# Performance work log

Hardware: AMD Instinct MI355X
Metric: run time of the kernel (lower is better)

The kernel has to match this reference:

```python
import jax, jax.numpy as jnp
import numpy as np

N, E = 12288, 196608
IN_DIM, HID, HEADS, EMB, K = 128, 256, 4, 16, 2
NEG_SLOPE = 0.2


def gat_layer(x, src, dst, W, a_s, a_d, b, heads, out_dim):
    # x: [N, Fin]; src/dst: [E'] (self-loops already appended)
    n = x.shape[0]
    h = (x @ W).reshape(n, heads, out_dim)                 # [N,H,F]
    alpha_src = jnp.einsum('nhf,hf->nh', h, a_s)           # [N,H]
    alpha_dst = jnp.einsum('nhf,hf->nh', h, a_d)
    e = jax.nn.leaky_relu(alpha_src[src] + alpha_dst[dst], NEG_SLOPE)  # [E,H]
    # softmax over incoming edges per destination node
    m = jax.ops.segment_max(e, dst, num_segments=n)
    ex = jnp.exp(e - m[dst])
    s = jax.ops.segment_sum(ex, dst, num_segments=n)
    alpha = ex / s[dst]                                    # [E,H]
    msg = h[src] * alpha[..., None]                        # [E,H,F]
    agg = jax.ops.segment_sum(msg, dst, num_segments=n)    # [N,H,F]
    return agg.reshape(n, heads * out_dim) + b


def setup_inputs() -> dict:
    key = jax.random.key(0)
    ks = jax.random.split(key, 16)
    x = jax.random.normal(ks[0], (N, IN_DIM), dtype=jnp.float32)
    edge_index = jax.random.randint(ks[1], (2, E), 0, N, dtype=jnp.int32)

    def glorot(k, shape):
        fan = shape[0] + shape[-1]
        return jax.random.normal(k, shape, dtype=jnp.float32) * jnp.sqrt(2.0 / fan)

    inp = {"x": x, "edge_index": edge_index}
    inp["W1"] = glorot(ks[2], (IN_DIM, HEADS * HID))
    inp["as1"] = glorot(ks[3], (HEADS, HID))
    inp["ad1"] = glorot(ks[4], (HEADS, HID))
    inp["b1"] = jnp.zeros((HEADS * HID,), jnp.float32)
    inp["W2"] = glorot(ks[5], (HEADS * HID, HEADS * HID))
    inp["as2"] = glorot(ks[6], (HEADS, HID))
    inp["ad2"] = glorot(ks[7], (HEADS, HID))
    inp["b2"] = jnp.zeros((HEADS * HID,), jnp.float32)
    # layer 3: 1024 -> 16, 1 head
    inp["W3"] = glorot(ks[8], (HEADS * HID, EMB))
    inp["as3"] = glorot(ks[9], (1, EMB))
    inp["ad3"] = glorot(ks[10], (1, EMB))
    inp["b3"] = jnp.zeros((EMB,), jnp.float32)
    inp["centers"] = jax.random.normal(ks[11], (K, EMB), dtype=jnp.float32)
    return inp


def reference(x, edge_index, W1, as1, ad1, b1, W2, as2, ad2, b2, W3, as3, ad3, b3, centers):
    n = x.shape[0]
    loop = jnp.arange(n, dtype=edge_index.dtype)
    src = jnp.concatenate([edge_index[0], loop])
    dst = jnp.concatenate([edge_index[1], loop])

    h = jax.nn.elu(gat_layer(x, src, dst, W1, as1, ad1, b1, HEADS, HID))
    h = jax.nn.elu(gat_layer(h, src, dst, W2, as2, ad2, b2, HEADS, HID))
    z = gat_layer(h, src, dst, W3, as3, ad3, b3, 1, EMB)   # [N,EMB]

    adj_recon = jax.nn.sigmoid(z @ z.T)                    # [N,N]

    # Student-t soft assignment
    d2 = jnp.sum((z[:, None, :] - centers[None, :, :]) ** 2, axis=2)  # [N,K]
    q = 1.0 / (1.0 + d2)
    q = q / jnp.sum(q, axis=1, keepdims=True)
    return z, adj_recon, q
```

## Files before the change

### kernel.cpp

```cpp
#include <hip/hip_runtime.h>
#include <hip/hip_bf16.h>
#include <math.h>

#define N_NODES 12288
#define N_EDGES 196608
#define EP_EDGES (N_EDGES + N_NODES)
#define HEADS 4
#define HID 256
#define FDIM 1024
#define EMB 16
#define NEG_SLOPE 0.2f

typedef __attribute__((ext_vector_type(8))) short short8;
typedef __attribute__((ext_vector_type(4))) float f32x4;

__device__ __forceinline__ unsigned short f2bf(float f) {
  unsigned int u = __float_as_uint(f);
  u = (u + 0x7FFFu + ((u >> 16) & 1u)) >> 16;
  return (unsigned short)u;
}
__device__ __forceinline__ float bf2f(unsigned short h) {
  return __uint_as_float(((unsigned int)h) << 16);
}

__device__ __forceinline__ void t_tile_hi(const float* __restrict__ W,
                                          unsigned short* __restrict__ Th,
                                          int K, int N, int k0, int n0,
                                          int t, float (*tile)[33]) {
  int rr = t >> 3, cc = (t & 7) * 4;
  float4 v = *reinterpret_cast<const float4*>(&W[(size_t)(k0 + rr) * N + n0 + cc]);
  tile[rr][cc + 0] = v.x; tile[rr][cc + 1] = v.y; tile[rr][cc + 2] = v.z; tile[rr][cc + 3] = v.w;
  __syncthreads();
  ushort4 h;
  h.x = f2bf(tile[cc + 0][rr]);
  h.y = f2bf(tile[cc + 1][rr]);
  h.z = f2bf(tile[cc + 2][rr]);
  h.w = f2bf(tile[cc + 3][rr]);
  *reinterpret_cast<ushort4*>(&Th[(size_t)(n0 + rr) * K + k0 + cc]) = h;
}

#define HIST_BLKS (EP_EDGES / 256)
__global__ __launch_bounds__(256) void k_hist_prep(const int* __restrict__ ei,
                                                   int* __restrict__ cnt,
                                                   const float* __restrict__ x,
                                                   unsigned short* __restrict__ xbf,
                                                   const float* __restrict__ W1,
                                                   unsigned short* __restrict__ w1tHi,
                                                   const float* __restrict__ W2,
                                                   unsigned short* __restrict__ w2tHi,
                                                   const float* __restrict__ as1,
                                                   const float* __restrict__ ad1,
                                                   float* __restrict__ wa,
                                                   const float* __restrict__ W3,
                                                   unsigned short* __restrict__ w3t) {
  __shared__ float tile[32][33];
  int b = blockIdx.x, t = threadIdx.x;
  if (b < HIST_BLKS) {
    int i = b * 256 + t;
    if (i < EP_EDGES) {
      int d = (i < N_EDGES) ? ei[N_EDGES + i] : (i - N_EDGES);
      atomicAdd(&cnt[d], 1);
    }
  } else if (b < HIST_BLKS + 1536) {
    int i = (b - HIST_BLKS) * 256 + t;
    float4 v = *reinterpret_cast<const float4*>(&x[(size_t)i * 4]);
    ushort4 h;
    h.x = f2bf(v.x); h.y = f2bf(v.y); h.z = f2bf(v.z); h.w = f2bf(v.w);
    *reinterpret_cast<ushort4*>(&xbf[(size_t)i * 4]) = h;
  } else if (b < HIST_BLKS + 1536 + 128) {
    int tt = b - HIST_BLKS - 1536;
    t_tile_hi(W1, w1tHi, 128, FDIM, (tt >> 5) * 32, (tt & 31) * 32, t, tile);
  } else if (b < HIST_BLKS + 1536 + 128 + 1024) {
    int tt = b - HIST_BLKS - 1536 - 128;
    t_tile_hi(W2, w2tHi, FDIM, FDIM, (tt >> 5) * 32, (tt & 31) * 32, t, tile);
  } else if (b == HIST_BLKS + 1536 + 128 + 1024) {
    for (int idx = t; idx < 1024; idx += 256) {
      int sd = idx >> 9, h = (idx >> 7) & 3, k = idx & 127;
      const float* av = sd ? ad1 : as1;
      float acc = 0.f;
      for (int f = 0; f < 256; ++f)
        acc = fmaf(W1[(size_t)k * FDIM + h * 256 + f], av[h * 256 + f], acc);
      wa[idx] = acc;
    }
  } else {
    for (int idx = t; idx < 16384; idx += 256) {
      int c = idx >> 10, k = idx & 1023;
      w3t[idx] = f2bf(W3[(size_t)k * 16 + c]);
    }
  }
}

__global__ __launch_bounds__(1024) void k_scan_alpha(const int* __restrict__ cnt,
                                                     int* __restrict__ row_ptr,
                                                     int* __restrict__ bsum,
                                                     const float* __restrict__ x,
                                                     const float* __restrict__ wa,
                                                     float* __restrict__ asrc,
                                                     float* __restrict__ adst) {
  __shared__ int sd[1024];
  int tid = threadIdx.x;
  if (blockIdx.x < 12) {
    int gid = blockIdx.x * 1024 + tid;
    int v = cnt[gid];
    sd[tid] = v;
    __syncthreads();
    for (int d = 1; d < 1024; d <<= 1) {
      int t2 = (tid >= d) ? sd[tid - d] : 0;
      __syncthreads();
      sd[tid] += t2;
      __syncthreads();
    }
    row_ptr[gid] = sd[tid] - v;
    if (tid == 1023) bsum[blockIdx.x] = sd[1023];
  } else {
    int id = (blockIdx.x - 12) * 1024 + tid;
    int n = id >> 2, h = id & 3;
    const float* wsv = wa + h * 128;
    const float* wdv = wa + 512 + h * 128;
    const float* xr = x + (size_t)n * 128;
    float accs = 0.f, accd = 0.f;
#pragma unroll
    for (int k = 0; k < 128; k += 4) {
      float4 xv = *reinterpret_cast<const float4*>(&xr[k]);
      float4 s4 = *reinterpret_cast<const float4*>(&wsv[k]);
      float4 d4 = *reinterpret_cast<const float4*>(&wdv[k]);
      accs = fmaf(xv.x, s4.x, fmaf(xv.y, s4.y, fmaf(xv.z, s4.z, fmaf(xv.w, s4.w, accs))));
      accd = fmaf(xv.x, d4.x, fmaf(xv.y, d4.y, fmaf(xv.z, d4.z, fmaf(xv.w, d4.w, accd))));
    }
    asrc[n * 4 + h] = accs;
    adst[n * 4 + h] = accd;
  }
}

__global__ void k_scan23(int* __restrict__ row_ptr, const int* __restrict__ bsum) {
  int gid = blockIdx.x * 256 + threadIdx.x;
  int blk = gid >> 10;
  int boffv = 0;
  for (int j = 0; j < blk; ++j) boffv += bsum[j];
  row_ptr[gid] += boffv;
  if (gid == 0) {
    int tot = 0;
    for (int j = 0; j < 12; ++j) tot += bsum[j];
    row_ptr[N_NODES] = tot;
  }
}

__global__ void k_scatter(const int* __restrict__ ei, const int* __restrict__ row_ptr,
                          int* __restrict__ cur, int* __restrict__ csr_src) {
  int i = blockIdx.x * 256 + threadIdx.x;
  if (i >= EP_EDGES) return;
  int s, d;
  if (i < N_EDGES) { s = ei[i]; d = ei[N_EDGES + i]; }
  else             { s = i - N_EDGES; d = s; }
  int pos = row_ptr[d] + atomicAdd(&cur[d], 1);
  csr_src[pos] = s;
}

__global__ __launch_bounds__(256) void k_aggx(const unsigned short* __restrict__ xbf,
                                              const float* __restrict__ asrc,
                                              const float* __restrict__ adst,
                                              const int* __restrict__ row_ptr,
                                              const int* __restrict__ csr_src,
                                              unsigned short* __restrict__ outHi) {
  int node = (blockIdx.x * 256 + threadIdx.x) >> 6;
  int lane = threadIdx.x & 63;
  int beg = row_ptr[node], end = row_ptr[node + 1];
  float4 adn = *reinterpret_cast<const float4*>(&adst[node * 4]);
  float m0 = -INFINITY, m1 = -INFINITY, m2 = -INFINITY, m3 = -INFINITY;
  float s0 = 0.f, s1 = 0.f, s2 = 0.f, s3 = 0.f;
  float a0x = 0.f, a0y = 0.f, a1x = 0.f, a1y = 0.f;
  float a2x = 0.f, a2y = 0.f, a3x = 0.f, a3y = 0.f;
  for (int e = beg; e < end; ++e) {
    int sidx = csr_src[e];
    float4 av = *reinterpret_cast<const float4*>(&asrc[sidx * 4]);
    ushort2 hu = *reinterpret_cast<const ushort2*>(&xbf[(size_t)sidx * 128 + lane * 2]);
    float hx = bf2f(hu.x), hy = bf2f(hu.y);
    float a, nm, sc, p;
    a = av.x + adn.x; a = a > 0.f ? a : NEG_SLOPE * a;
    nm = fmaxf(m0, a); sc = __expf(m0 - nm); p = __expf(a - nm); m0 = nm;
    s0 = s0 * sc + p; a0x = a0x * sc + p * hx; a0y = a0y * sc + p * hy;
    a = av.y + adn.y; a = a > 0.f ? a : NEG_SLOPE * a;
    nm = fmaxf(m1, a); sc = __expf(m1 - nm); p = __expf(a - nm); m1 = nm;
    s1 = s1 * sc + p; a1x = a1x * sc + p * hx; a1y = a1y * sc + p * hy;
    a = av.z + adn.z; a = a > 0.f ? a : NEG_SLOPE * a;
    nm = fmaxf(m2, a); sc = __expf(m2 - nm); p = __expf(a - nm); m2 = nm;
    s2 = s2 * sc + p; a2x = a2x * sc + p * hx; a2y = a2y * sc + p * hy;
    a = av.w + adn.w; a = a > 0.f ? a : NEG_SLOPE * a;
    nm = fmaxf(m3, a); sc = __expf(m3 - nm); p = __expf(a - nm); m3 = nm;
    s3 = s3 * sc + p; a3x = a3x * sc + p * hx; a3y = a3y * sc + p * hy;
  }
  size_t base = (size_t)node * 512 + lane * 2;
  ushort2 o;
  float inv;
  inv = 1.f / s0; o.x = f2bf(a0x * inv); o.y = f2bf(a0y * inv);
  *reinterpret_cast<ushort2*>(&outHi[base + 0 * 128]) = o;
  inv = 1.f / s1; o.x = f2bf(a1x * inv); o.y = f2bf(a1y * inv);
  *reinterpret_cast<ushort2*>(&outHi[base + 1 * 128]) = o;
  inv = 1.f / s2; o.x = f2bf(a2x * inv); o.y = f2bf(a2y * inv);
  *reinterpret_cast<ushort2*>(&outHi[base + 2 * 128]) = o;
  inv = 1.f / s3; o.x = f2bf(a3x * inv); o.y = f2bf(a3y * inv);
  *reinterpret_cast<ushort2*>(&outHi[base + 3 * 128]) = o;
}

template <int MODE>
__global__ __launch_bounds__(256) void k_gemm(const unsigned short* __restrict__ A,
                                              const unsigned short* __restrict__ B,
                                              unsigned short* __restrict__ Out,
                                              const float* __restrict__ bias,
                                              const float* __restrict__ a_s,
                                              const float* __restrict__ a_d,
                                              float* __restrict__ asrcP,
                                              float* __restrict__ adstP,
                                              int M, int N, int K, int lda) {
  __shared__ unsigned short sA[128 * 32], sB[128 * 32];
  const int tid = threadIdx.x;
  const int lane = tid & 63, wv = tid >> 6;
  const int row0 = blockIdx.y * 128, col0 = blockIdx.x * 128;
  const int mBase = (wv >> 1) * 64, nBase = (wv & 1) * 64;
  const int lane15 = lane & 15;
  const int aoff = (MODE == 1) ? (col0 >> 8) * 128 : 0;

  f32x4 acc[4][4];
#pragma unroll
  for (int m = 0; m < 4; ++m)
#pragma unroll
    for (int n = 0; n < 4; ++n) acc[m][n] = (f32x4){0.f, 0.f, 0.f, 0.f};

  int rS[2], cS[2], dS[2];
#pragma unroll
  for (int c = 0; c < 2; ++c) {
    int p = c * 4096 + tid * 16;
    int r = p >> 6, u = (p >> 4) & 3;
    int f = (r & 3) ^ ((r >> 2) & 3);
    rS[c] = r; cS[c] = (u ^ f) * 8; dS[c] = c * 2048 + tid * 8;
  }
  const int fR = (lane & 3) ^ ((lane >> 2) & 3);
  const int uprime = (((lane >> 4) ^ fR) * 8);

  for (int k0 = 0; k0 < K; k0 += 32) {
#pragma unroll
    for (int c = 0; c < 2; ++c) {
      size_t ga = (size_t)(row0 + rS[c]) * lda + aoff + k0 + cS[c];
      size_t gb = (size_t)(col0 + rS[c]) * K + k0 + cS[c];
      __builtin_amdgcn_global_load_lds((const __attribute__((address_space(1))) void*)(A + ga),
                                       (__attribute__((address_space(3))) void*)(sA + dS[c]), 16, 0, 0);
      __builtin_amdgcn_global_load_lds((const __attribute__((address_space(1))) void*)(B + gb),
                                       (__attribute__((address_space(3))) void*)(sB + dS[c]), 16, 0, 0);
    }
    __syncthreads();

    short8 a[4], b[4];
#pragma unroll
    for (int m = 0; m < 4; ++m) {
      int ia = (mBase + m * 16 + lane15) * 32 + uprime;
      a[m] = *reinterpret_cast<const short8*>(sA + ia);
      int ib = (nBase + m * 16 + lane15) * 32 + uprime;
      b[m] = *reinterpret_cast<const short8*>(sB + ib);
    }
#pragma unroll
    for (int m = 0; m < 4; ++m)
#pragma unroll
      for (int n = 0; n < 4; ++n)
        acc[m][n] = __builtin_amdgcn_mfma_f32_16x16x32_bf16(a[m], b[n], acc[m][n], 0, 0, 0);
    __syncthreads();
  }

  const int head = col0 >> 8;
  const int q = ((col0 >> 6) & 2) | (nBase >> 6);
  float asv[4], adv[4];
  if (MODE == 0) {
#pragma unroll
    for (int n = 0; n < 4; ++n) {
      int cc = col0 + nBase + n * 16 + lane15;
      asv[n] = a_s[cc];
      adv[n] = a_d[cc];
    }
  }

#pragma unroll
  for (int m = 0; m < 4; ++m) {
    int rr = row0 + mBase + m * 16 + (lane >> 4) * 4;
#pragma unroll
    for (int j = 0; j < 4; ++j) {
      if (MODE == 1) {
#pragma unroll
        for (int n = 0; n < 4; ++n) {
          int cc = col0 + nBase + n * 16 + lane15;
          float v = acc[m][n][j] + bias[cc];
          v = v > 0.f ? v : __expf(v) - 1.f;
          Out[(size_t)(rr + j) * N + cc] = f2bf(v);
        }
      } else {
        float ps = 0.f, pd = 0.f;
#pragma unroll
        for (int n = 0; n < 4; ++n) {
          int cc = col0 + nBase + n * 16 + lane15;
          float v = acc[m][n][j];
          Out[(size_t)(rr + j) * N + cc] = f2bf(v);
          ps = fmaf(v, asv[n], ps);
          pd = fmaf(v, adv[n], pd);
        }
        ps += __shfl_xor(ps, 1); pd += __shfl_xor(pd, 1);
        ps += __shfl_xor(ps, 2); pd += __shfl_xor(pd, 2);
        ps += __shfl_xor(ps, 4); pd += __shfl_xor(pd, 4);
        ps += __shfl_xor(ps, 8); pd += __shfl_xor(pd, 8);
        if (lane15 == 0) {
          asrcP[(size_t)(rr + j) * 16 + head * 4 + q] = ps;
          adstP[(size_t)(rr + j) * 16 + head * 4 + q] = pd;
        }
      }
    }
  }
}

__global__ __launch_bounds__(256) void k_agg4(const unsigned short* __restrict__ h,
                                              const float* __restrict__ asrcP,
                                              const float* __restrict__ adstP,
                                              const int* __restrict__ row_ptr,
                                              const int* __restrict__ csr_src, const float* __restrict__ bias,
                                              unsigned short* __restrict__ outHi) {
  int wid = (blockIdx.x * 256 + threadIdx.x) >> 6;
  int lane = threadIdx.x & 63;
  int node = wid >> 2, hd = wid & 3;
  int beg = row_ptr[node], end = row_ptr[node + 1];
  float4 dq = *reinterpret_cast<const float4*>(&adstP[(size_t)node * 16 + hd * 4]);
  float adn = dq.x + dq.y + dq.z + dq.w;
  float m = -INFINITY, s = 0.f;
  float ax = 0.f, ay = 0.f, az = 0.f, aw = 0.f;
  for (int e = beg; e < end; ++e) {
    int sidx = csr_src[e];
    float4 sq = *reinterpret_cast<const float4*>(&asrcP[(size_t)sidx * 16 + hd * 4]);
    float a = (sq.x + sq.y + sq.z + sq.w) + adn;
    a = a > 0.f ? a : NEG_SLOPE * a;
    float nm = fmaxf(m, a);
    float sc = __expf(m - nm);
    float p  = __expf(a - nm);
    m = nm;
    s = s * sc + p;
    ushort4 hu = *reinterpret_cast<const ushort4*>(&h[(size_t)sidx * FDIM + hd * HID + lane * 4]);
    ax = ax * sc + p * bf2f(hu.x);
    ay = ay * sc + p * bf2f(hu.y);
    az = az * sc + p * bf2f(hu.z);
    aw = aw * sc + p * bf2f(hu.w);
  }
  float inv = 1.f / s;
  int fo = hd * HID + lane * 4;
  float4 bv = *reinterpret_cast<const float4*>(&bias[fo]);
  float4 o;
  o.x = ax * inv + bv.x; o.y = ay * inv + bv.y; o.z = az * inv + bv.z; o.w = aw * inv + bv.w;
  o.x = o.x > 0.f ? o.x : __expf(o.x) - 1.f;
  o.y = o.y > 0.f ? o.y : __expf(o.y) - 1.f;
  o.z = o.z > 0.f ? o.z : __expf(o.z) - 1.f;
  o.w = o.w > 0.f ? o.w : __expf(o.w) - 1.f;
  ushort4 hh;
  hh.x = f2bf(o.x); hh.y = f2bf(o.y); hh.z = f2bf(o.z); hh.w = f2bf(o.w);
  *reinterpret_cast<ushort4*>(&outHi[(size_t)node * FDIM + fo]) = hh;
}

__global__ __launch_bounds__(256) void k_gemm_n16(const unsigned short* __restrict__ A,
                                                  const unsigned short* __restrict__ w3t,
                                                  const float* __restrict__ a_s,
                                                  const float* __restrict__ a_d,
                                                  float* __restrict__ C,
                                                  float* __restrict__ asrc,
                                                  float* __restrict__ adst) {
  int wave = (blockIdx.x * 256 + threadIdx.x) >> 6;
  int lane = threadIdx.x & 63;
  int lane15 = lane & 15;
  int row0 = wave * 16;
  int kg = (lane >> 4) * 8;
  f32x4 acc = (f32x4){0.f, 0.f, 0.f, 0.f};
  const unsigned short* Ar = A + (size_t)(row0 + lane15) * FDIM + kg;
  const unsigned short* Br = w3t + (size_t)lane15 * FDIM + kg;
  for (int k0 = 0; k0 < FDIM; k0 += 32) {
    short8 a = *reinterpret_cast<const short8*>(Ar + k0);
    short8 b = *reinterpret_cast<const short8*>(Br + k0);
    acc = __builtin_amdgcn_mfma_f32_16x16x32_bf16(a, b, acc, 0, 0, 0);
  }
  float asv = a_s[lane15], adv = a_d[lane15];
  int rbase = row0 + (lane >> 4) * 4;
#pragma unroll
  for (int j = 0; j < 4; ++j) {
    float v = acc[j];
    C[(size_t)(rbase + j) * EMB + lane15] = v;
    float ps = v * asv, pd = v * adv;
    ps += __shfl_xor(ps, 1); pd += __shfl_xor(pd, 1);
    ps += __shfl_xor(ps, 2); pd += __shfl_xor(pd, 2);
    ps += __shfl_xor(ps, 4); pd += __shfl_xor(pd, 4);
    ps += __shfl_xor(ps, 8); pd += __shfl_xor(pd, 8);
    if (lane15 == 0) { asrc[rbase + j] = ps; adst[rbase + j] = pd; }
  }
}

__global__ __launch_bounds__(256) void k_agg1(const float* __restrict__ h3, const float* __restrict__ asrc,
                                              const float* __restrict__ adst, const int* __restrict__ row_ptr,
                                              const int* __restrict__ csr_src, const float* __restrict__ bias,
                                              const float* __restrict__ centers,
                                              float* __restrict__ z, float* __restrict__ qout) {
  int idx = blockIdx.x * 256 + threadIdx.x;
  int node = idx >> 4, f = idx & 15;
  if (node >= N_NODES) return;
  int beg = row_ptr[node], end = row_ptr[node + 1];
  float adn = adst[node];
  float m = -INFINITY, s = 0.f, acc = 0.f;
  for (int e = beg; e < end; ++e) {
    int sidx = csr_src[e];
    float a = asrc[sidx] + adn;
    a = a > 0.f ? a : NEG_SLOPE * a;
    float nm = fmaxf(m, a);
    float sc = __expf(m - nm);
    float p  = __expf(a - nm);
    m = nm;
    s = s * sc + p;
    acc = acc * sc + p * h3[sidx * EMB + f];
  }
  float zv = acc / s + bias[f];
  z[node * EMB + f] = zv;
  float d0 = zv - centers[f];       d0 *= d0;
  float d1 = zv - centers[EMB + f]; d1 *= d1;
  d0 += __shfl_xor(d0, 1); d1 += __shfl_xor(d1, 1);
  d0 += __shfl_xor(d0, 2); d1 += __shfl_xor(d1, 2);
  d0 += __shfl_xor(d0, 4); d1 += __shfl_xor(d1, 4);
  d0 += __shfl_xor(d0, 8); d1 += __shfl_xor(d1, 8);
  if (f == 0) {
    float q0 = 1.f / (1.f + d0), q1 = 1.f / (1.f + d1);
    float inv = 1.f / (q0 + q1);
    qout[node * 2 + 0] = q0 * inv;
    qout[node * 2 + 1] = q1 * inv;
  }
}

__global__ __launch_bounds__(256) void k_adj(const float* __restrict__ z, float* __restrict__ adj) {
  __shared__ float Zr[16][64];
  __shared__ float Zc[16][64];
  int tid = threadIdx.x;
  int r0 = blockIdx.y * 64, c0 = blockIdx.x * 64;
  {
    int m = tid >> 2, kk = (tid & 3) * 4;
    float4 v = *reinterpret_cast<const float4*>(&z[(size_t)(r0 + m) * EMB + kk]);
    Zr[kk + 0][m] = v.x; Zr[kk + 1][m] = v.y; Zr[kk + 2][m] = v.z; Zr[kk + 3][m] = v.w;
    float4 w = *reinterpret_cast<const float4*>(&z[(size_t)(c0 + m) * EMB + kk]);
    Zc[kk + 0][m] = w.x; Zc[kk + 1][m] = w.y; Zc[kk + 2][m] = w.z; Zc[kk + 3][m] = w.w;
  }
  __syncthreads();
  int tx = tid & 15, ty = tid >> 4;
  float acc[4][4] = {};
#pragma unroll
  for (int k = 0; k < 16; ++k) {
    float a[4], b[4];
#pragma unroll
    for (int i = 0; i < 4; ++i) a[i] = Zr[k][ty * 4 + i];
#pragma unroll
    for (int j = 0; j < 4; ++j) b[j] = Zc[k][tx * 4 + j];
#pragma unroll
    for (int i = 0; i < 4; ++i)
#pragma unroll
      for (int j = 0; j < 4; ++j) acc[i][j] = fmaf(a[i], b[j], acc[i][j]);
  }
  for (int i = 0; i < 4; ++i) {
    float4 o;
    o.x = 1.f / (1.f + __expf(-acc[i][0]));
    o.y = 1.f / (1.f + __expf(-acc[i][1]));
    o.z = 1.f / (1.f + __expf(-acc[i][2]));
    o.w = 1.f / (1.f + __expf(-acc[i][3]));
    *reinterpret_cast<float4*>(&adj[(size_t)(r0 + ty * 4 + i) * N_NODES + c0 + tx * 4]) = o;
  }
}

extern "C" void kernel_launch(void* const* d_in, const int* in_sizes, int n_in,
                              void* d_out, int out_size, void* d_ws, size_t ws_size,
                              hipStream_t stream) {
  const float* x   = (const float*)d_in[0];
  const int*   ei  = (const int*)d_in[1];
  const float* W1  = (const float*)d_in[2];
  const float* as1 = (const float*)d_in[3];
  const float* ad1 = (const float*)d_in[4];
  const float* b1  = (const float*)d_in[5];
  const float* W2  = (const float*)d_in[6];
  const float* as2 = (const float*)d_in[7];
  const float* ad2 = (const float*)d_in[8];
  const float* b2  = (const float*)d_in[9];
  const float* W3  = (const float*)d_in[10];
  const float* as3 = (const float*)d_in[11];
  const float* ad3 = (const float*)d_in[12];
  const float* b3  = (const float*)d_in[13];
  const float* centers = (const float*)d_in[14];
  float* out = (float*)d_out;

  char* ws = (char*)d_ws;
  size_t off = 0;
  auto alloc = [&](size_t bytes) { void* p = ws + off; off = (off + bytes + 255) & ~(size_t)255; return p; };
  int* cnt       = (int*)alloc((size_t)N_NODES * 4);
  int* cur       = (int*)alloc((size_t)N_NODES * 4);
  int* row_ptr   = (int*)alloc((size_t)(N_NODES + 1) * 4);
  int* bsum      = (int*)alloc(64 * 4);
  int* csr_src   = (int*)alloc((size_t)EP_EDGES * 4);
  float* asrcA   = (float*)alloc((size_t)N_NODES * HEADS * 4);
  float* adstA   = (float*)alloc((size_t)N_NODES * HEADS * 4);
  float* asrcP   = (float*)alloc((size_t)N_NODES * 16 * 4);
  float* adstP   = (float*)alloc((size_t)N_NODES * 16 * 4);
  float* asrc3   = (float*)alloc((size_t)N_NODES * 4);
  float* adst3   = (float*)alloc((size_t)N_NODES * 4);
  float* wa      = (float*)alloc(1024 * 4);
  unsigned short* xbf    = (unsigned short*)alloc((size_t)N_NODES * 128 * 2);
  unsigned short* aggxHi = (unsigned short*)alloc((size_t)N_NODES * 512 * 2);
  unsigned short* h1bf   = (unsigned short*)alloc((size_t)N_NODES * FDIM * 2);
  unsigned short* hbf    = (unsigned short*)alloc((size_t)N_NODES * FDIM * 2);
  unsigned short* agg2Hi = (unsigned short*)alloc((size_t)N_NODES * FDIM * 2);
  unsigned short* w1tHi  = (unsigned short*)alloc((size_t)FDIM * 128 * 2);
  unsigned short* w2tHi  = (unsigned short*)alloc((size_t)FDIM * FDIM * 2);
  unsigned short* w3t    = (unsigned short*)alloc((size_t)16 * FDIM * 2);
  float* bufZ    = (float*)alloc((size_t)N_NODES * EMB * 4);

  hipMemsetAsync(cnt, 0, (size_t)N_NODES * 8, stream);

  k_hist_prep<<<dim3(HIST_BLKS + 1536 + 128 + 1024 + 2), dim3(256), 0, stream>>>(
      ei, cnt, x, xbf, W1, w1tHi, W2, w2tHi, as1, ad1, wa, W3, w3t);

  k_scan_alpha<<<dim3(12 + 48), dim3(1024), 0, stream>>>(
      cnt, row_ptr, bsum, x, wa, asrcA, adstA);

  k_scan23<<<dim3(N_NODES / 256), dim3(256), 0, stream>>>(row_ptr, bsum);
  k_scatter<<<dim3((EP_EDGES + 255) / 256), dim3(256), 0, stream>>>(ei, row_ptr, cur, csr_src);

  k_aggx<<<dim3(N_NODES / 4), dim3(256), 0, stream>>>(xbf, asrcA, adstA, row_ptr, csr_src, aggxHi);
  k_gemm<1><<<dim3(FDIM / 128, N_NODES / 128), dim3(256), 0, stream>>>(
      aggxHi, w1tHi, h1bf, b1, nullptr, nullptr, nullptr, nullptr, N_NODES, FDIM, 128, 512);

  k_gemm<0><<<dim3(FDIM / 128, N_NODES / 128), dim3(256), 0, stream>>>(
      h1bf, w2tHi, hbf, nullptr, as2, ad2, asrcP, adstP, N_NODES, FDIM, FDIM, FDIM);
  k_agg4<<<dim3(N_NODES), dim3(256), 0, stream>>>(hbf, asrcP, adstP, row_ptr, csr_src, b2, agg2Hi);

  k_gemm_n16<<<dim3(N_NODES / 64), dim3(256), 0, stream>>>(
      agg2Hi, w3t, as3, ad3, bufZ, asrc3, adst3);
  float* adj = out + (size_t)N_NODES * EMB;
  float* q   = adj + (size_t)N_NODES * N_NODES;
  k_agg1<<<dim3(N_NODES * EMB / 256), dim3(256), 0, stream>>>(
      bufZ, asrc3, adst3, row_ptr, csr_src, b3, centers, out, q);

  k_adj<<<dim3(N_NODES / 64, N_NODES / 64), dim3(256), 0, stream>>>(out, adj);
}
```

Measured before the change: 453.2 us.

## Gather layer-2 features as FP8 and compute z·zᵀ with split-bf16 MFMA

Adds a repack kernel that converts the bf16 layer-2 features to packed FP8, so the edge-gather aggregation reads a quarter of the bytes per neighbor instead of half. The adjacency reconstruction kernel now uses bf16 MFMA on a hi/lo split of z, written by the layer-3 aggregation, instead of scalar FP32 FMAs from shared memory, with larger 128x128 tiles. FP8 storage of the hidden features loses a lot of precision and may exceed the tolerance. The extra repack pass also adds a full read and write of the feature matrix.

```diff
diff --git a/kernel.cpp b/kernel.cpp
--- a/kernel.cpp
+++ b/kernel.cpp
@@ -13,6 +13,7 @@
 
 typedef __attribute__((ext_vector_type(8))) short short8;
 typedef __attribute__((ext_vector_type(4))) float f32x4;
+typedef __attribute__((ext_vector_type(2))) float f32x2;
 
 __device__ __forceinline__ unsigned short f2bf(float f) {
   unsigned int u = __float_as_uint(f);
@@ -313,7 +314,16 @@
   }
 }
 
-__global__ __launch_bounds__(256) void k_agg4(const unsigned short* __restrict__ h,
+__global__ void k_repack8(const unsigned short* __restrict__ hbf,
+                          unsigned int* __restrict__ h8) {
+  int i = blockIdx.x * 256 + threadIdx.x;
+  ushort4 v = *reinterpret_cast<const ushort4*>(&hbf[(size_t)i * 4]);
+  int w = __builtin_amdgcn_cvt_pk_fp8_f32(bf2f(v.x), bf2f(v.y), 0, false);
+  w = __builtin_amdgcn_cvt_pk_fp8_f32(bf2f(v.z), bf2f(v.w), w, true);
+  h8[i] = (unsigned int)w;
+}
+
+__global__ __launch_bounds__(256) void k_agg4(const unsigned int* __restrict__ h8,
                                               const float* __restrict__ asrcP,
                                               const float* __restrict__ adstP,
                                               const int* __restrict__ row_ptr,
@@ -337,11 +347,13 @@
     float p  = __expf(a - nm);
     m = nm;
     s = s * sc + p;
-    ushort4 hu = *reinterpret_cast<const ushort4*>(&h[(size_t)sidx * FDIM + hd * HID + lane * 4]);
-    ax = ax * sc + p * bf2f(hu.x);
-    ay = ay * sc + p * bf2f(hu.y);
-    az = az * sc + p * bf2f(hu.z);
-    aw = aw * sc + p * bf2f(hu.w);
+    unsigned int dw = h8[(size_t)sidx * 256 + hd * 64 + lane];
+    f32x2 lo = __builtin_amdgcn_cvt_pk_f32_fp8(dw, false);
+    f32x2 hi = __builtin_amdgcn_cvt_pk_f32_fp8(dw, true);
+    ax = ax * sc + p * lo.x;
+    ay = ay * sc + p * lo.y;
+    az = az * sc + p * hi.x;
+    aw = aw * sc + p * hi.y;
   }
   float inv = 1.f / s;
   int fo = hd * HID + lane * 4;
@@ -396,7 +408,9 @@
                                               const float* __restrict__ adst, const int* __restrict__ row_ptr,
                                               const int* __restrict__ csr_src, const float* __restrict__ bias,
                                               const float* __restrict__ centers,
-                                              float* __restrict__ z, float* __restrict__ qout) {
+                                              float* __restrict__ z, float* __restrict__ qout,
+                                              unsigned short* __restrict__ zh,
+                                              unsigned short* __restrict__ zl) {
   int idx = blockIdx.x * 256 + threadIdx.x;
   int node = idx >> 4, f = idx & 15;
   if (node >= N_NODES) return;
@@ -416,6 +430,9 @@
   }
   float zv = acc / s + bias[f];
   z[node * EMB + f] = zv;
+  unsigned short hv = f2bf(zv);
+  zh[node * EMB + f] = hv;
+  zl[node * EMB + f] = f2bf(zv - bf2f(hv));
   float d0 = zv - centers[f];       d0 *= d0;
   float d1 = zv - centers[EMB + f]; d1 *= d1;
   d0 += __shfl_xor(d0, 1); d1 += __shfl_xor(d1, 1);
@@ -430,40 +447,48 @@
   }
 }
 
-__global__ __launch_bounds__(256) void k_adj(const float* __restrict__ z, float* __restrict__ adj) {
-  __shared__ float Zr[16][64];
-  __shared__ float Zc[16][64];
+__global__ __launch_bounds__(256) void k_adj(const unsigned short* __restrict__ zh,
+                                             const unsigned short* __restrict__ zl,
+                                             float* __restrict__ adj) {
   int tid = threadIdx.x;
-  int r0 = blockIdx.y * 64, c0 = blockIdx.x * 64;
-  {
-    int m = tid >> 2, kk = (tid & 3) * 4;
-    float4 v = *reinterpret_cast<const float4*>(&z[(size_t)(r0 + m) * EMB + kk]);
-    Zr[kk + 0][m] = v.x; Zr[kk + 1][m] = v.y; Zr[kk + 2][m] = v.z; Zr[kk + 3][m] = v.w;
-    float4 w = *reinterpret_cast<const float4*>(&z[(size_t)(c0 + m) * EMB + kk]);
-    Zc[kk + 0][m] = w.x; Zc[kk + 1][m] = w.y; Zc[kk + 2][m] = w.z; Zc[kk + 3][m] = w.w;
-  }
-  __syncthreads();
-  int tx = tid & 15, ty = tid >> 4;
-  float acc[4][4] = {};
-#pragma unroll
-  for (int k = 0; k < 16; ++k) {
-    float a[4], b[4];
-#pragma unroll
-    for (int i = 0; i < 4; ++i) a[i] = Zr[k][ty * 4 + i];
-#pragma unroll
-    for (int j = 0; j < 4; ++j) b[j] = Zc[k][tx * 4 + j];
-#pragma unroll
-    for (int i = 0; i < 4; ++i)
-#pragma unroll
-      for (int j = 0; j < 4; ++j) acc[i][j] = fmaf(a[i], b[j], acc[i][j]);
-  }
-  for (int i = 0; i < 4; ++i) {
-    float4 o;
-    o.x = 1.f / (1.f + __expf(-acc[i][0]));
-    o.y = 1.f / (1.f + __expf(-acc[i][1]));
-    o.z = 1.f / (1.f + __expf(-acc[i][2]));
-    o.w = 1.f / (1.f + __expf(-acc[i][3]));
-    *reinterpret_cast<float4*>(&adj[(size_t)(r0 + ty * 4 + i) * N_NODES + c0 + tx * 4]) = o;
+  int lane = tid & 63, wv = tid >> 6;
+  int r0 = blockIdx.y * 128 + wv * 32, c0 = blockIdx.x * 128;
+  int l15 = lane & 15, kg = lane >> 4;
+  short8 zero = (short8){0, 0, 0, 0, 0, 0, 0, 0};
+  short8 ah[2], al[2];
+#pragma unroll
+  for (int g = 0; g < 2; ++g) {
+    int row = r0 + g * 16 + l15;
+    if (kg < 2) {
+      ah[g] = *reinterpret_cast<const short8*>(&zh[(size_t)row * EMB + kg * 8]);
+      al[g] = *reinterpret_cast<const short8*>(&zl[(size_t)row * EMB + kg * 8]);
+    } else { ah[g] = zero; al[g] = zero; }
+  }
+  short8 bh[8], bl[8];
+#pragma unroll
+  for (int n = 0; n < 8; ++n) {
+    int col = c0 + n * 16 + l15;
+    if (kg < 2) {
+      bh[n] = *reinterpret_cast<const short8*>(&zh[(size_t)col * EMB + kg * 8]);
+      bl[n] = *reinterpret_cast<const short8*>(&zl[(size_t)col * EMB + kg * 8]);
+    } else { bh[n] = zero; bl[n] = zero; }
+  }
+#pragma unroll
+  for (int g = 0; g < 2; ++g) {
+    int rbase = r0 + g * 16 + kg * 4;
+#pragma unroll
+    for (int n = 0; n < 8; ++n) {
+      f32x4 acc = (f32x4){0.f, 0.f, 0.f, 0.f};
+      acc = __builtin_amdgcn_mfma_f32_16x16x32_bf16(ah[g], bh[n], acc, 0, 0, 0);
+      acc = __builtin_amdgcn_mfma_f32_16x16x32_bf16(ah[g], bl[n], acc, 0, 0, 0);
+      acc = __builtin_amdgcn_mfma_f32_16x16x32_bf16(al[g], bh[n], acc, 0, 0, 0);
+      int cc = c0 + n * 16 + l15;
+#pragma unroll
+      for (int j = 0; j < 4; ++j) {
+        float v = 1.f / (1.f + __expf(-acc[j]));
+        adj[(size_t)(rbase + j) * N_NODES + cc] = v;
+      }
+    }
   }
 }
 
@@ -506,10 +531,13 @@
   unsigned short* aggxHi = (unsigned short*)alloc((size_t)N_NODES * 512 * 2);
   unsigned short* h1bf   = (unsigned short*)alloc((size_t)N_NODES * FDIM * 2);
   unsigned short* hbf    = (unsigned short*)alloc((size_t)N_NODES * FDIM * 2);
+  unsigned int*   h8     = (unsigned int*)alloc((size_t)N_NODES * FDIM);
   unsigned short* agg2Hi = (unsigned short*)alloc((size_t)N_NODES * FDIM * 2);
   unsigned short* w1tHi  = (unsigned short*)alloc((size_t)FDIM * 128 * 2);
   unsigned short* w2tHi  = (unsigned short*)alloc((size_t)FDIM * FDIM * 2);
   unsigned short* w3t    = (unsigned short*)alloc((size_t)16 * FDIM * 2);
+  unsigned short* zh     = (unsigned short*)alloc((size_t)N_NODES * EMB * 2);
+  unsigned short* zl     = (unsigned short*)alloc((size_t)N_NODES * EMB * 2);
   float* bufZ    = (float*)alloc((size_t)N_NODES * EMB * 4);
 
   hipMemsetAsync(cnt, 0, (size_t)N_NODES * 8, stream);
@@ -529,14 +557,15 @@
 
   k_gemm<0><<<dim3(FDIM / 128, N_NODES / 128), dim3(256), 0, stream>>>(
       h1bf, w2tHi, hbf, nullptr, as2, ad2, asrcP, adstP, N_NODES, FDIM, FDIM, FDIM);
-  k_agg4<<<dim3(N_NODES), dim3(256), 0, stream>>>(hbf, asrcP, adstP, row_ptr, csr_src, b2, agg2Hi);
+  k_repack8<<<dim3(N_NODES * FDIM / 4 / 256), dim3(256), 0, stream>>>(hbf, h8);
+  k_agg4<<<dim3(N_NODES), dim3(256), 0, stream>>>(h8, asrcP, adstP, row_ptr, csr_src, b2, agg2Hi);
 
   k_gemm_n16<<<dim3(N_NODES / 64), dim3(256), 0, stream>>>(
       agg2Hi, w3t, as3, ad3, bufZ, asrc3, adst3);
   float* adj = out + (size_t)N_NODES * EMB;
   float* q   = adj + (size_t)N_NODES * N_NODES;
   k_agg1<<<dim3(N_NODES * EMB / 256), dim3(256), 0, stream>>>(
-      bufZ, asrc3, adst3, row_ptr, csr_src, b3, centers, out, q);
-
-  k_adj<<<dim3(N_NODES / 64, N_NODES / 64), dim3(256), 0, stream>>>(out, adj);
-}
+      bufZ, asrc3, adst3, row_ptr, csr_src, b3, centers, out, q, zh, zl);
+
+  k_adj<<<dim3(N_NODES / 128, N_NODES / 128), dim3(256), 0, stream>>>(zh, zl, adj);
+}
```

Measured after the change: 441.2 us. -2.7%, faster.
